# Performance work log

Measured on AMD Instinct MI355X. Metric: run time of the kernel, lower is better.

Reference implementation:

```python
import jax, jax.numpy as jnp
import numpy as np

N = 100000
E = 1600000

def _norms(src, dst):
    ones = jnp.ones(src.shape[0], dtype=jnp.float32)
    out_deg = jax.ops.segment_sum(ones, src, num_segments=N)
    in_deg = jax.ops.segment_sum(ones, dst, num_segments=N)
    # dgl clamps degree to >=1; with self-loops deg>=1 anyway
    out_norm = jax.lax.rsqrt(jnp.clip(out_deg, 1.0))
    in_norm = jax.lax.rsqrt(jnp.clip(in_deg, 1.0))
    return out_norm, in_norm

def _graph_conv(x, W, b, src, dst, out_norm, in_norm):
    h = (x * out_norm[:, None]) @ W          # [N, dout]
    msg = h[src]                              # gather  [E', dout]
    agg = jax.ops.segment_sum(msg, dst, num_segments=N)
    return agg * in_norm[:, None] + b

def setup_inputs() -> dict:
    key = jax.random.key(0)
    ks = jax.random.split(key, 8)
    feat = jax.random.normal(ks[0], (N, 128), dtype=jnp.float32)
    src = jax.random.randint(ks[1], (E,), 0, N, dtype=jnp.int32)
    dst = jax.random.randint(ks[2], (E,), 0, N, dtype=jnp.int32)
    s1 = 1.0 / np.sqrt(128.0)
    W1 = jax.random.uniform(ks[3], (128, 128), jnp.float32, -s1, s1)
    b1 = jnp.zeros((128,), jnp.float32)
    W2 = jax.random.uniform(ks[4], (128, 128), jnp.float32, -s1, s1)
    b2 = jnp.zeros((128,), jnp.float32)
    W3 = jax.random.uniform(ks[5], (128, 64), jnp.float32, -s1, s1)
    b3 = jnp.zeros((64,), jnp.float32)
    return {"feat": feat, "src": src, "dst": dst,
            "W1": W1, "b1": b1, "W2": W2, "b2": b2, "W3": W3, "b3": b3}

def reference(feat, src, dst, W1, b1, W2, b2, W3, b3):
    # dgl.add_self_loop
    loop = jnp.arange(N, dtype=src.dtype)
    s = jnp.concatenate([src, loop])
    d = jnp.concatenate([dst, loop])
    out_norm, in_norm = _norms(s, d)
    # dropout is identity in eval mode (deterministic reference)
    h = jax.nn.relu(_graph_conv(feat, W1, b1, s, d, out_norm, in_norm))
    h = jax.nn.relu(_graph_conv(h, W2, b2, s, d, out_norm, in_norm))
    h = _graph_conv(h, W3, b3, s, d, out_norm, in_norm)
    return h
```

## Files before the change

### kernel.cpp

```cpp
#include <hip/hip_runtime.h>
#include <hip/hip_fp16.h>


#define NFEAT 128
#define BBITS 8
#define BSZ 256
#define EPB 4096

union H8 { float4 f4; __half2 h2[4]; };

using half8v = __attribute__((ext_vector_type(8))) _Float16;
using f32x4  = __attribute__((ext_vector_type(4))) float;

__global__ __launch_bounds__(256) void hist_kernel(const int* __restrict__ src,
                                                   const int* __restrict__ dst,
                                                   int* __restrict__ hist2,
                                                   int NB, int nblk, int nh, int E) {
    __shared__ int hd[512], hs[512];
    const int t = threadIdx.x, b = blockIdx.x;
    for (int u = t; u < 512; u += 256) { hd[u] = 0; hs[u] = 0; }
    __syncthreads();
    const int base4 = b * (EPB / 4);
    #pragma unroll
    for (int j = 0; j < 4; ++j) {
        int i4 = base4 + j * 256 + t;
        int e0 = i4 * 4;
        if (e0 + 3 < E) {
            int4 s = ((const int4*)src)[i4];
            int4 d = ((const int4*)dst)[i4];
            atomicAdd(&hs[s.x >> BBITS], 1); atomicAdd(&hs[s.y >> BBITS], 1);
            atomicAdd(&hs[s.z >> BBITS], 1); atomicAdd(&hs[s.w >> BBITS], 1);
            atomicAdd(&hd[d.x >> BBITS], 1); atomicAdd(&hd[d.y >> BBITS], 1);
            atomicAdd(&hd[d.z >> BBITS], 1); atomicAdd(&hd[d.w >> BBITS], 1);
        } else {
            for (int e = e0; e < E && e < e0 + 4; ++e) {
                atomicAdd(&hs[src[e] >> BBITS], 1);
                atomicAdd(&hd[dst[e] >> BBITS], 1);
            }
        }
    }
    __syncthreads();
    for (int u = t; u < NB; u += 256) {
        hist2[u * nblk + b]      = hd[u];
        hist2[nh + u * nblk + b] = hs[u];
    }
}

__global__ __launch_bounds__(256) void scan1_kernel(int* __restrict__ data,
                                                    int* __restrict__ blk_sum, int n) {
    const int tid = threadIdx.x, lane = tid & 63, wid = tid >> 6;
    const int i2 = blockIdx.x * 256 + tid;
    int a = 0, b = 0;
    if (2 * i2 + 1 < n)      { int2 v = ((const int2*)data)[i2]; a = v.x; b = v.y; }
    else if (2 * i2 < n)     { a = data[2 * i2]; }
    int s = a + b;
    int incl = s;
    #pragma unroll
    for (int off = 1; off < 64; off <<= 1) {
        int t2 = __shfl_up(incl, off, 64);
        if (lane >= off) incl += t2;
    }
    __shared__ int ws[4];
    if (lane == 63) ws[wid] = incl;
    __syncthreads();
    int woff = 0;
    #pragma unroll
    for (int w = 0; w < 3; ++w) if (w < wid) woff += ws[w];
    int pref = woff + incl - s;
    if (2 * i2 < n)     data[2 * i2]     = pref;
    if (2 * i2 + 1 < n) data[2 * i2 + 1] = pref + a;
    if (tid == 0) blk_sum[blockIdx.x] = ws[0] + ws[1] + ws[2] + ws[3];
}

__global__ __launch_bounds__(1024) void scan2_kernel(int* __restrict__ blk, int nb) {
    const int tid = threadIdx.x, lane = tid & 63, wid = tid >> 6;
    int v = (tid < nb) ? blk[tid] : 0;
    int incl = v;
    #pragma unroll
    for (int off = 1; off < 64; off <<= 1) {
        int t = __shfl_up(incl, off, 64);
        if (lane >= off) incl += t;
    }
    __shared__ int ws[16];
    if (lane == 63) ws[wid] = incl;
    __syncthreads();
    int woff = 0;
    #pragma unroll
    for (int w = 0; w < 15; ++w) if (w < wid) woff += ws[w];
    if (tid < nb) blk[tid] = woff + incl - v;
}

__global__ __launch_bounds__(256) void scan3_kernel(int* __restrict__ data,
                                                    const int* __restrict__ blk, int n) {
    const int i2 = blockIdx.x * 256 + threadIdx.x;
    int add = blk[blockIdx.x];
    if (2 * i2 < n)     data[2 * i2]     += add;
    if (2 * i2 + 1 < n) data[2 * i2 + 1] += add;
}

__global__ __launch_bounds__(512) void scatter_kernel(const int* __restrict__ src,
                                                      const int* __restrict__ dst,
                                                      const int* __restrict__ hist2,
                                                      unsigned int* __restrict__ dstP,
                                                      unsigned char* __restrict__ srcB,
                                                      int NB, int nblk, int nh, int E) {
    __shared__ int hd[512], hs[512], startD[512], startS[512], baseD[512], baseS[512];
    __shared__ int ws[8];
    __shared__ unsigned int   payD[EPB];
    __shared__ unsigned short kD[EPB];
    __shared__ unsigned char  sV[EPB];
    __shared__ unsigned short kS[EPB];
    const int t = threadIdx.x, b = blockIdx.x;
    const int lane = t & 63, wid = t >> 6;
    hd[t] = 0; hs[t] = 0;
    for (int u = t; u < NB; u += 512) {
        baseD[u] = hist2[u * nblk + b];
        baseS[u] = hist2[nh + u * nblk + b] - E;
    }
    __syncthreads();

    const int e0 = b * EPB;
    const int nE = min(EPB, E - e0);
    int se[8], de[8], rD[8], rS[8];
    const int be = e0 + t * 8;
    if (be + 7 < E) {
        int4 s0 = ((const int4*)src)[(be >> 2)];
        int4 s1 = ((const int4*)src)[(be >> 2) + 1];
        int4 d0 = ((const int4*)dst)[(be >> 2)];
        int4 d1 = ((const int4*)dst)[(be >> 2) + 1];
        se[0]=s0.x; se[1]=s0.y; se[2]=s0.z; se[3]=s0.w;
        se[4]=s1.x; se[5]=s1.y; se[6]=s1.z; se[7]=s1.w;
        de[0]=d0.x; de[1]=d0.y; de[2]=d0.z; de[3]=d0.w;
        de[4]=d1.x; de[5]=d1.y; de[6]=d1.z; de[7]=d1.w;
    } else {
        #pragma unroll
        for (int j = 0; j < 8; ++j) {
            se[j] = (be + j < E) ? src[be + j] : 0;
            de[j] = (be + j < E) ? dst[be + j] : 0;
        }
    }
    #pragma unroll
    for (int j = 0; j < 8; ++j) {
        if (be + j < E) {
            rD[j] = atomicAdd(&hd[de[j] >> BBITS], 1);
            rS[j] = atomicAdd(&hs[se[j] >> BBITS], 1);
        }
    }
    __syncthreads();
    {
        int v = hd[t], incl = v;
        #pragma unroll
        for (int o = 1; o < 64; o <<= 1) {
            int x = __shfl_up(incl, o, 64);
            if (lane >= o) incl += x;
        }
        if (lane == 63) ws[wid] = incl;
        __syncthreads();
        int woff = 0;
        #pragma unroll
        for (int w = 0; w < 7; ++w) if (w < wid) woff += ws[w];
        startD[t] = woff + incl - v;
    }
    __syncthreads();
    {
        int v = hs[t], incl = v;
        #pragma unroll
        for (int o = 1; o < 64; o <<= 1) {
            int x = __shfl_up(incl, o, 64);
            if (lane >= o) incl += x;
        }
        if (lane == 63) ws[wid] = incl;
        __syncthreads();
        int woff = 0;
        #pragma unroll
        for (int w = 0; w < 7; ++w) if (w < wid) woff += ws[w];
        startS[t] = woff + incl - v;
    }
    __syncthreads();
    #pragma unroll
    for (int j = 0; j < 8; ++j) {
        if (be + j < E) {
            int kd = de[j] >> BBITS;
            int p  = startD[kd] + rD[j];
            payD[p] = ((unsigned int)(de[j] & (BSZ - 1)) << 24) | (unsigned int)se[j];
            kD[p]   = (unsigned short)kd;
            int ks = se[j] >> BBITS;
            int q  = startS[ks] + rS[j];
            sV[q] = (unsigned char)(se[j] & (BSZ - 1));
            kS[q] = (unsigned short)ks;
        }
    }
    __syncthreads();
    for (int p = t; p < nE; p += 512) {
        int k = kD[p];
        dstP[baseD[k] + (p - startD[k])] = payD[p];
        int k2 = kS[p];
        srcB[baseS[k2] + (p - startS[k2])] = sV[p];
    }
}

__global__ __launch_bounds__(256) void bucket_kernel(const unsigned int* __restrict__ dstP,
                                                     const unsigned char* __restrict__ srcB,
                                                     const int* __restrict__ hist2,
                                                     int* __restrict__ row_ptr,
                                                     int* __restrict__ col_idx,
                                                     float* __restrict__ in_norm,
                                                     float* __restrict__ out_norm,
                                                     int N, int NB, int nblk, int nh, int E) {
    __shared__ int cnt[BSZ], scnt[BSZ], start[BSZ], off[BSZ];
    __shared__ int ws[4];
    const int k = blockIdx.x, t = threadIdx.x;
    const int node0 = k << BBITS;
    cnt[t] = 0; scnt[t] = 0; off[t] = 0;
    __syncthreads();
    const int bB = hist2[k * nblk];
    const int bE = (k + 1 < NB) ? hist2[(k + 1) * nblk] : E;
    const int sB = hist2[nh + k * nblk] - E;
    const int sE = ((k + 1 < NB) ? hist2[nh + (k + 1) * nblk] : 2 * E) - E;
    for (int i = bB + t; i < bE; i += 256) atomicAdd(&cnt[dstP[i] >> 24], 1);
    for (int i = sB + t; i < sE; i += 256) atomicAdd(&scnt[srcB[i]], 1);
    __syncthreads();
    const int lane = t & 63, wid = t >> 6;
    int v = cnt[t];
    int incl = v;
    #pragma unroll
    for (int o = 1; o < 64; o <<= 1) {
        int x = __shfl_up(incl, o, 64);
        if (lane >= o) incl += x;
    }
    if (lane == 63) ws[wid] = incl;
    __syncthreads();
    int woff = 0;
    #pragma unroll
    for (int w = 0; w < 3; ++w) if (w < wid) woff += ws[w];
    start[t] = woff + incl - v;
    {
        int node = node0 + t;
        if (node < N) {
            row_ptr[node] = bB + start[t];
            in_norm[node]  = rsqrtf((float)(v + 1));
            out_norm[node] = rsqrtf((float)(scnt[t] + 1));
        }
    }
    if (k == 0 && t == 0) row_ptr[N] = E;
    __syncthreads();
    for (int i = bB + t; i < bE; i += 256) {
        unsigned int pv = dstP[i];
        int local = pv >> 24;
        int r = atomicAdd(&off[local], 1);
        col_idx[bB + start[local] + r] = (int)(pv & 0xFFFFFFu);
    }
}

__global__ void wt_all_kernel(const float* __restrict__ W1, const float* __restrict__ W2,
                              const float* __restrict__ W3, __half* __restrict__ Wt1,
                              __half* __restrict__ Wt2, __half* __restrict__ Wt3) {
    int b = blockIdx.x, k = threadIdx.x;
    if (b < 128)      Wt1[b * 128 + k] = __float2half(W1[k * 128 + b]);
    else if (b < 256) { int n = b - 128; Wt2[n * 128 + k] = __float2half(W2[k * 128 + n]); }
    else              { int n = b - 256; Wt3[n * 128 + k] = __float2half(W3[k * 64 + n]); }
}

template <int BN, typename XT>
__global__ __launch_bounds__(256) void mfma_gemm_kernel(const XT* __restrict__ x,
                                                        const __half* __restrict__ Wt,
                                                        const float* __restrict__ out_norm,
                                                        __half* __restrict__ h, int n_rows) {
    constexpr int BM = 64;
    constexpr int NT = BN / 16;
    __shared__ __half As[BM][136];
    __shared__ __half Bs[BN][136];
    const int tid  = threadIdx.x;
    const int row0 = blockIdx.x * BM;

    {
        int r  = tid >> 2;
        int c0 = (tid & 3) * 32;
        int grow = row0 + r;
        if (grow < n_rows) {
            float norm = out_norm[grow];
            if constexpr (sizeof(XT) == 4) {
                const float* xp = (const float*)x + (size_t)grow * NFEAT + c0;
                #pragma unroll
                for (int j = 0; j < 4; ++j) {
                    float4 p0 = *(const float4*)(xp + j * 8);
                    float4 p1 = *(const float4*)(xp + j * 8 + 4);
                    H8 u;
                    u.h2[0] = __floats2half2_rn(p0.x * norm, p0.y * norm);
                    u.h2[1] = __floats2half2_rn(p0.z * norm, p0.w * norm);
                    u.h2[2] = __floats2half2_rn(p1.x * norm, p1.y * norm);
                    u.h2[3] = __floats2half2_rn(p1.z * norm, p1.w * norm);
                    *(float4*)&As[r][c0 + j * 8] = u.f4;
                }
            } else {
                const __half* xp = (const __half*)x + (size_t)grow * NFEAT + c0;
                #pragma unroll
                for (int j = 0; j < 4; ++j) {
                    H8 u; u.f4 = *(const float4*)(xp + j * 8);
                    #pragma unroll
                    for (int q = 0; q < 4; ++q) {
                        float2 p = __half22float2(u.h2[q]);
                        u.h2[q] = __floats2half2_rn(p.x * norm, p.y * norm);
                    }
                    *(float4*)&As[r][c0 + j * 8] = u.f4;
                }
            }
        } else {
            H8 z; z.f4 = make_float4(0.f, 0.f, 0.f, 0.f);
            #pragma unroll
            for (int j = 0; j < 4; ++j) *(float4*)&As[r][c0 + j * 8] = z.f4;
        }
    }
    {
        constexpr int TPR = 256 / BN;
        constexpr int CH  = 128 / TPR;
        int wr = tid / TPR;
        int wc = (tid % TPR) * CH;
        const __half* wp = Wt + wr * 128 + wc;
        #pragma unroll
        for (int j = 0; j < CH / 8; ++j)
            *(float4*)&Bs[wr][wc + j * 8] = *(const float4*)(wp + j * 8);
    }
    __syncthreads();

    const int lane = tid & 63, wid = tid >> 6;
    const int lr = lane & 15, quad = lane >> 4;
    const int koff = quad * 8;
    f32x4 acc[NT];
    #pragma unroll
    for (int t = 0; t < NT; ++t) acc[t] = (f32x4){0.f, 0.f, 0.f, 0.f};

    #pragma unroll
    for (int ks = 0; ks < 4; ++ks) {
        half8v a = *(const half8v*)&As[wid * 16 + lr][ks * 32 + koff];
        #pragma unroll
        for (int nt = 0; nt < NT; ++nt) {
            half8v b = *(const half8v*)&Bs[nt * 16 + lr][ks * 32 + koff];
            acc[nt] = __builtin_amdgcn_mfma_f32_16x16x32_f16(a, b, acc[nt], 0, 0, 0);
        }
    }

    #pragma unroll
    for (int nt = 0; nt < NT; ++nt) {
        #pragma unroll
        for (int r = 0; r < 4; ++r) {
            int row = row0 + wid * 16 + quad * 4 + r;
            if (row < n_rows)
                h[(size_t)row * BN + nt * 16 + lr] = __float2half(acc[nt][r]);
        }
    }
}

template <int DOUT, bool RELU, typename OutT>
__global__ __launch_bounds__(256) void agg_kernel(const __half* __restrict__ h,
                                                  const int* __restrict__ row_ptr,
                                                  const int* __restrict__ col_idx,
                                                  const float* __restrict__ in_norm,
                                                  const float* __restrict__ bias,
                                                  OutT* __restrict__ out, int n) {
    constexpr int TPN = DOUT / 8;
    constexpr int NPB = 256 / TPN;
    const int tid  = threadIdx.x;
    const int sub  = tid / TPN;
    const int c    = (tid % TPN) * 8;
    const int node = blockIdx.x * NPB + sub;
    if (node >= n) return;

    float acc[8];
    {
        H8 u; u.f4 = *(const float4*)(h + (size_t)node * DOUT + c);
        #pragma unroll
        for (int q = 0; q < 4; ++q) {
            float2 p = __half22float2(u.h2[q]);
            acc[q * 2] = p.x; acc[q * 2 + 1] = p.y;
        }
    }
    int e  = row_ptr[node];
    int e1 = row_ptr[node + 1];
    for (; e + 3 < e1; e += 4) {
        int s0 = col_idx[e], s1 = col_idx[e + 1], s2 = col_idx[e + 2], s3 = col_idx[e + 3];
        H8 u0, u1, u2, u3;
        u0.f4 = *(const float4*)(h + (size_t)s0 * DOUT + c);
        u1.f4 = *(const float4*)(h + (size_t)s1 * DOUT + c);
        u2.f4 = *(const float4*)(h + (size_t)s2 * DOUT + c);
        u3.f4 = *(const float4*)(h + (size_t)s3 * DOUT + c);
        #pragma unroll
        for (int q = 0; q < 4; ++q) {
            float2 p0 = __half22float2(u0.h2[q]);
            float2 p1 = __half22float2(u1.h2[q]);
            float2 p2 = __half22float2(u2.h2[q]);
            float2 p3 = __half22float2(u3.h2[q]);
            acc[q * 2]     += (p0.x + p1.x) + (p2.x + p3.x);
            acc[q * 2 + 1] += (p0.y + p1.y) + (p2.y + p3.y);
        }
    }
    for (; e < e1; ++e) {
        int s0 = col_idx[e];
        H8 u0; u0.f4 = *(const float4*)(h + (size_t)s0 * DOUT + c);
        #pragma unroll
        for (int q = 0; q < 4; ++q) {
            float2 p0 = __half22float2(u0.h2[q]);
            acc[q * 2] += p0.x; acc[q * 2 + 1] += p0.y;
        }
    }
    float inn = in_norm[node];
    float r[8];
    #pragma unroll
    for (int q = 0; q < 8; ++q) {
        r[q] = acc[q] * inn + bias[c + q];
        if (RELU) r[q] = fmaxf(r[q], 0.0f);
    }
    if constexpr (sizeof(OutT) == 2) {
        H8 o;
        #pragma unroll
        for (int q = 0; q < 4; ++q) o.h2[q] = __floats2half2_rn(r[q * 2], r[q * 2 + 1]);
        *(float4*)((__half*)out + (size_t)node * DOUT + c) = o.f4;
    } else {
        float4 o0, o1;
        o0.x=r[0]; o0.y=r[1]; o0.z=r[2]; o0.w=r[3];
        o1.x=r[4]; o1.y=r[5]; o1.z=r[6]; o1.w=r[7];
        *(float4*)((float*)out + (size_t)node * DOUT + c)     = o0;
        *(float4*)((float*)out + (size_t)node * DOUT + c + 4) = o1;
    }
}

extern "C" void kernel_launch(void* const* d_in, const int* in_sizes, int n_in,
                              void* d_out, int out_size, void* d_ws, size_t ws_size,
                              hipStream_t stream) {
    const float* feat = (const float*)d_in[0];
    const int*   src  = (const int*)d_in[1];
    const int*   dst  = (const int*)d_in[2];
    const float* W1   = (const float*)d_in[3];
    const float* b1   = (const float*)d_in[4];
    const float* W2   = (const float*)d_in[5];
    const float* b2   = (const float*)d_in[6];
    const float* W3   = (const float*)d_in[7];
    const float* b3   = (const float*)d_in[8];

    const int N = in_sizes[0] / NFEAT;
    const int E = in_sizes[1];

    const int NB   = (N + BSZ - 1) / BSZ;
    const int nblk = (E + EPB - 1) / EPB;
    const int nh   = NB * nblk;
    const int n2   = 2 * nh;
    const int nsb  = (n2 + 511) / 512;

    char* ws = (char*)d_ws;
    auto alloc = [&](size_t bytes) {
        char* p = ws;
        ws += (bytes + 255) & ~(size_t)255;
        return p;
    };
    float* out_norm = (float*)alloc((size_t)N * 4);
    float* in_norm  = (float*)alloc((size_t)N * 4);
    int*   row_ptr  = (int*)alloc((size_t)(N + 1) * 4);
    int*   hist2    = (int*)alloc((size_t)n2 * 4);
    int*   blk_sum  = (int*)alloc((size_t)1024 * 4);
    __half* Wt1     = (__half*)alloc((size_t)128 * 128 * 2);
    __half* Wt2     = (__half*)alloc((size_t)128 * 128 * 2);
    __half* Wt3     = (__half*)alloc((size_t)64 * 128 * 2);
    int*   col_idx  = (int*)alloc((size_t)E * 4);
    __half* hA      = (__half*)alloc((size_t)N * NFEAT * 2);
    __half* hB      = (__half*)alloc((size_t)N * NFEAT * 2);
    unsigned int*  dstP = (unsigned int*)hA;
    unsigned char* srcB = (unsigned char*)(dstP + E);

    wt_all_kernel<<<320, 128, 0, stream>>>(W1, W2, W3, Wt1, Wt2, Wt3);

    hist_kernel<<<nblk, 256, 0, stream>>>(src, dst, hist2, NB, nblk, nh, E);
    scan1_kernel<<<nsb, 256, 0, stream>>>(hist2, blk_sum, n2);
    scan2_kernel<<<1, 1024, 0, stream>>>(blk_sum, nsb);
    scan3_kernel<<<nsb, 256, 0, stream>>>(hist2, blk_sum, n2);
    scatter_kernel<<<nblk, 512, 0, stream>>>(src, dst, hist2, dstP, srcB, NB, nblk, nh, E);
    bucket_kernel<<<NB, 256, 0, stream>>>(dstP, srcB, hist2, row_ptr, col_idx,
                                          in_norm, out_norm, N, NB, nblk, nh, E);

    const int gb = (N + 63) / 64;
    mfma_gemm_kernel<128, float><<<gb, 256, 0, stream>>>(feat, Wt1, out_norm, hA, N);
    agg_kernel<128, true, __half><<<(N + 15) / 16, 256, 0, stream>>>(hA, row_ptr, col_idx,
                                                                     in_norm, b1, hB, N);
    mfma_gemm_kernel<128, __half><<<gb, 256, 0, stream>>>(hB, Wt2, out_norm, hA, N);
    agg_kernel<128, true, __half><<<(N + 15) / 16, 256, 0, stream>>>(hA, row_ptr, col_idx,
                                                                     in_norm, b2, hB, N);
    mfma_gemm_kernel<64, __half><<<gb, 256, 0, stream>>>(hB, Wt3, out_norm, hA, N);
    agg_kernel<64, false, float><<<(N + 31) / 32, 256, 0, stream>>>(hA, row_ptr, col_idx,
                                                                    in_norm, b3, (float*)d_out, N);
}
```

Baseline: 345.9 us.

## Fuse aggregation of layers 1-2 with the following layer's GEMM

The layer-1 and layer-2 aggregation (gather-sum, norm, bias, ReLU, out_norm scaling) now writes its half-precision result straight into shared memory, and the next layer's MFMA GEMM runs in the same kernel. This removes two launches and the global write and re-read of the intermediate N x 128 activation. In exchange, each fused block handles 64 nodes with 16 threads per node over four serial passes, which may reduce memory-level parallelism for the irregular gathers, and blocks with high-degree nodes can stall the GEMM.

```diff
diff --git a/kernel.cpp b/kernel.cpp
--- a/kernel.cpp
+++ b/kernel.cpp
@@ -261,17 +261,15 @@
     else              { int n = b - 256; Wt3[n * 128 + k] = __float2half(W3[k * 64 + n]); }
 }
 
-template <int BN, typename XT>
-__global__ __launch_bounds__(256) void mfma_gemm_kernel(const XT* __restrict__ x,
+__global__ __launch_bounds__(256) void mfma_gemm_kernel(const float* __restrict__ x,
                                                         const __half* __restrict__ Wt,
                                                         const float* __restrict__ out_norm,
                                                         __half* __restrict__ h, int n_rows) {
-    constexpr int BM = 64;
-    constexpr int NT = BN / 16;
-    __shared__ __half As[BM][136];
+    constexpr int BN = 128, NT = BN / 16;
+    __shared__ __half As[64][136];
     __shared__ __half Bs[BN][136];
     const int tid  = threadIdx.x;
-    const int row0 = blockIdx.x * BM;
+    const int row0 = blockIdx.x * 64;
 
     {
         int r  = tid >> 2;
@@ -279,31 +277,17 @@
         int grow = row0 + r;
         if (grow < n_rows) {
             float norm = out_norm[grow];
-            if constexpr (sizeof(XT) == 4) {
-                const float* xp = (const float*)x + (size_t)grow * NFEAT + c0;
-                #pragma unroll
-                for (int j = 0; j < 4; ++j) {
-                    float4 p0 = *(const float4*)(xp + j * 8);
-                    float4 p1 = *(const float4*)(xp + j * 8 + 4);
-                    H8 u;
-                    u.h2[0] = __floats2half2_rn(p0.x * norm, p0.y * norm);
-                    u.h2[1] = __floats2half2_rn(p0.z * norm, p0.w * norm);
-                    u.h2[2] = __floats2half2_rn(p1.x * norm, p1.y * norm);
-                    u.h2[3] = __floats2half2_rn(p1.z * norm, p1.w * norm);
-                    *(float4*)&As[r][c0 + j * 8] = u.f4;
-                }
-            } else {
-                const __half* xp = (const __half*)x + (size_t)grow * NFEAT + c0;
-                #pragma unroll
-                for (int j = 0; j < 4; ++j) {
-                    H8 u; u.f4 = *(const float4*)(xp + j * 8);
-                    #pragma unroll
-                    for (int q = 0; q < 4; ++q) {
-                        float2 p = __half22float2(u.h2[q]);
-                        u.h2[q] = __floats2half2_rn(p.x * norm, p.y * norm);
-                    }
-                    *(float4*)&As[r][c0 + j * 8] = u.f4;
-                }
+            const float* xp = x + (size_t)grow * NFEAT + c0;
+            #pragma unroll
+            for (int j = 0; j < 4; ++j) {
+                float4 p0 = *(const float4*)(xp + j * 8);
+                float4 p1 = *(const float4*)(xp + j * 8 + 4);
+                H8 u;
+                u.h2[0] = __floats2half2_rn(p0.x * norm, p0.y * norm);
+                u.h2[1] = __floats2half2_rn(p0.z * norm, p0.w * norm);
+                u.h2[2] = __floats2half2_rn(p1.x * norm, p1.y * norm);
+                u.h2[3] = __floats2half2_rn(p1.z * norm, p1.w * norm);
+                *(float4*)&As[r][c0 + j * 8] = u.f4;
             }
         } else {
             H8 z; z.f4 = make_float4(0.f, 0.f, 0.f, 0.f);
@@ -312,6 +296,56 @@
         }
     }
     {
+        int wr = tid / 2;
+        int wc = (tid % 2) * 64;
+        const __half* wp = Wt + wr * 128 + wc;
+        #pragma unroll
+        for (int j = 0; j < 8; ++j)
+            *(float4*)&Bs[wr][wc + j * 8] = *(const float4*)(wp + j * 8);
+    }
+    __syncthreads();
+
+    const int lane = tid & 63, wid = tid >> 6;
+    const int lr = lane & 15, quad = lane >> 4;
+    const int koff = quad * 8;
+    f32x4 acc[NT];
+    #pragma unroll
+    for (int t = 0; t < NT; ++t) acc[t] = (f32x4){0.f, 0.f, 0.f, 0.f};
+
+    #pragma unroll
+    for (int ks = 0; ks < 4; ++ks) {
+        half8v a = *(const half8v*)&As[wid * 16 + lr][ks * 32 + koff];
+        #pragma unroll
+        for (int nt = 0; nt < NT; ++nt) {
+            half8v b = *(const half8v*)&Bs[nt * 16 + lr][ks * 32 + koff];
+            acc[nt] = __builtin_amdgcn_mfma_f32_16x16x32_f16(a, b, acc[nt], 0, 0, 0);
+        }
+    }
+
+    #pragma unroll
+    for (int nt = 0; nt < NT; ++nt) {
+        #pragma unroll
+        for (int r = 0; r < 4; ++r) {
+            int row = row0 + wid * 16 + quad * 4 + r;
+            if (row < n_rows)
+                h[(size_t)row * BN + nt * 16 + lr] = __float2half(acc[nt][r]);
+        }
+    }
+}
+
+template <int BN>
+__global__ __launch_bounds__(256) void fused_agg_gemm_kernel(
+        const __half* __restrict__ hin, const int* __restrict__ row_ptr,
+        const int* __restrict__ col_idx, const float* __restrict__ in_norm,
+        const float* __restrict__ out_norm, const float* __restrict__ bias,
+        const __half* __restrict__ Wt, __half* __restrict__ hout, int n) {
+    constexpr int NT = BN / 16;
+    __shared__ __half As[64][136];
+    __shared__ __half Bs[BN][136];
+    const int tid   = threadIdx.x;
+    const int node0 = blockIdx.x * 64;
+
+    {
         constexpr int TPR = 256 / BN;
         constexpr int CH  = 128 / TPR;
         int wr = tid / TPR;
@@ -321,6 +355,66 @@
         for (int j = 0; j < CH / 8; ++j)
             *(float4*)&Bs[wr][wc + j * 8] = *(const float4*)(wp + j * 8);
     }
+
+    const int sub = tid >> 4;
+    const int c   = (tid & 15) * 8;
+    #pragma unroll
+    for (int p = 0; p < 4; ++p) {
+        const int nl   = p * 16 + sub;
+        const int node = node0 + nl;
+        if (node < n) {
+            float acc[8];
+            {
+                H8 u; u.f4 = *(const float4*)(hin + (size_t)node * 128 + c);
+                #pragma unroll
+                for (int q = 0; q < 4; ++q) {
+                    float2 pp = __half22float2(u.h2[q]);
+                    acc[q * 2] = pp.x; acc[q * 2 + 1] = pp.y;
+                }
+            }
+            int e  = row_ptr[node];
+            int e1 = row_ptr[node + 1];
+            for (; e + 3 < e1; e += 4) {
+                int s0 = col_idx[e], s1 = col_idx[e + 1];
+                int s2 = col_idx[e + 2], s3 = col_idx[e + 3];
+                H8 u0, u1, u2, u3;
+                u0.f4 = *(const float4*)(hin + (size_t)s0 * 128 + c);
+                u1.f4 = *(const float4*)(hin + (size_t)s1 * 128 + c);
+                u2.f4 = *(const float4*)(hin + (size_t)s2 * 128 + c);
+                u3.f4 = *(const float4*)(hin + (size_t)s3 * 128 + c);
+                #pragma unroll
+                for (int q = 0; q < 4; ++q) {
+                    float2 p0 = __half22float2(u0.h2[q]);
+                    float2 p1 = __half22float2(u1.h2[q]);
+                    float2 p2 = __half22float2(u2.h2[q]);
+                    float2 p3 = __half22float2(u3.h2[q]);
+                    acc[q * 2]     += (p0.x + p1.x) + (p2.x + p3.x);
+                    acc[q * 2 + 1] += (p0.y + p1.y) + (p2.y + p3.y);
+                }
+            }
+            for (; e < e1; ++e) {
+                int s0 = col_idx[e];
+                H8 u0; u0.f4 = *(const float4*)(hin + (size_t)s0 * 128 + c);
+                #pragma unroll
+                for (int q = 0; q < 4; ++q) {
+                    float2 p0 = __half22float2(u0.h2[q]);
+                    acc[q * 2] += p0.x; acc[q * 2 + 1] += p0.y;
+                }
+            }
+            float inn = in_norm[node], onorm = out_norm[node];
+            H8 o;
+            #pragma unroll
+            for (int q = 0; q < 4; ++q) {
+                float r0 = fmaxf(acc[q * 2]     * inn + bias[c + q * 2],     0.0f) * onorm;
+                float r1 = fmaxf(acc[q * 2 + 1] * inn + bias[c + q * 2 + 1], 0.0f) * onorm;
+                o.h2[q] = __floats2half2_rn(r0, r1);
+            }
+            *(float4*)&As[nl][c] = o.f4;
+        } else {
+            H8 z; z.f4 = make_float4(0.f, 0.f, 0.f, 0.f);
+            *(float4*)&As[nl][c] = z.f4;
+        }
+    }
     __syncthreads();
 
     const int lane = tid & 63, wid = tid >> 6;
@@ -344,22 +438,20 @@
     for (int nt = 0; nt < NT; ++nt) {
         #pragma unroll
         for (int r = 0; r < 4; ++r) {
-            int row = row0 + wid * 16 + quad * 4 + r;
-            if (row < n_rows)
-                h[(size_t)row * BN + nt * 16 + lr] = __float2half(acc[nt][r]);
-        }
-    }
-}
-
-template <int DOUT, bool RELU, typename OutT>
-__global__ __launch_bounds__(256) void agg_kernel(const __half* __restrict__ h,
-                                                  const int* __restrict__ row_ptr,
-                                                  const int* __restrict__ col_idx,
-                                                  const float* __restrict__ in_norm,
-                                                  const float* __restrict__ bias,
-                                                  OutT* __restrict__ out, int n) {
-    constexpr int TPN = DOUT / 8;
-    constexpr int NPB = 256 / TPN;
+            int row = node0 + wid * 16 + quad * 4 + r;
+            if (row < n)
+                hout[(size_t)row * BN + nt * 16 + lr] = __float2half(acc[nt][r]);
+        }
+    }
+}
+
+__global__ __launch_bounds__(256) void agg64_kernel(const __half* __restrict__ h,
+                                                    const int* __restrict__ row_ptr,
+                                                    const int* __restrict__ col_idx,
+                                                    const float* __restrict__ in_norm,
+                                                    const float* __restrict__ bias,
+                                                    float* __restrict__ out, int n) {
+    constexpr int DOUT = 64, TPN = DOUT / 8, NPB = 256 / TPN;
     const int tid  = threadIdx.x;
     const int sub  = tid / TPN;
     const int c    = (tid % TPN) * 8;
@@ -404,24 +496,13 @@
         }
     }
     float inn = in_norm[node];
-    float r[8];
-    #pragma unroll
-    for (int q = 0; q < 8; ++q) {
-        r[q] = acc[q] * inn + bias[c + q];
-        if (RELU) r[q] = fmaxf(r[q], 0.0f);
-    }
-    if constexpr (sizeof(OutT) == 2) {
-        H8 o;
-        #pragma unroll
-        for (int q = 0; q < 4; ++q) o.h2[q] = __floats2half2_rn(r[q * 2], r[q * 2 + 1]);
-        *(float4*)((__half*)out + (size_t)node * DOUT + c) = o.f4;
-    } else {
-        float4 o0, o1;
-        o0.x=r[0]; o0.y=r[1]; o0.z=r[2]; o0.w=r[3];
-        o1.x=r[4]; o1.y=r[5]; o1.z=r[6]; o1.w=r[7];
-        *(float4*)((float*)out + (size_t)node * DOUT + c)     = o0;
-        *(float4*)((float*)out + (size_t)node * DOUT + c + 4) = o1;
-    }
+    float4 o0, o1;
+    o0.x = acc[0] * inn + bias[c + 0]; o0.y = acc[1] * inn + bias[c + 1];
+    o0.z = acc[2] * inn + bias[c + 2]; o0.w = acc[3] * inn + bias[c + 3];
+    o1.x = acc[4] * inn + bias[c + 4]; o1.y = acc[5] * inn + bias[c + 5];
+    o1.z = acc[6] * inn + bias[c + 6]; o1.w = acc[7] * inn + bias[c + 7];
+    *(float4*)(out + (size_t)node * DOUT + c)     = o0;
+    *(float4*)(out + (size_t)node * DOUT + c + 4) = o1;
 }
 
 extern "C" void kernel_launch(void* const* d_in, const int* in_sizes, int n_in,
@@ -477,13 +558,11 @@
                                           in_norm, out_norm, N, NB, nblk, nh, E);
 
     const int gb = (N + 63) / 64;
-    mfma_gemm_kernel<128, float><<<gb, 256, 0, stream>>>(feat, Wt1, out_norm, hA, N);
-    agg_kernel<128, true, __half><<<(N + 15) / 16, 256, 0, stream>>>(hA, row_ptr, col_idx,
-                                                                     in_norm, b1, hB, N);
-    mfma_gemm_kernel<128, __half><<<gb, 256, 0, stream>>>(hB, Wt2, out_norm, hA, N);
-    agg_kernel<128, true, __half><<<(N + 15) / 16, 256, 0, stream>>>(hA, row_ptr, col_idx,
-                                                                     in_norm, b2, hB, N);
-    mfma_gemm_kernel<64, __half><<<gb, 256, 0, stream>>>(hB, Wt3, out_norm, hA, N);
-    agg_kernel<64, false, float><<<(N + 31) / 32, 256, 0, stream>>>(hA, row_ptr, col_idx,
-                                                                    in_norm, b3, (float*)d_out, N);
-}
+    mfma_gemm_kernel<<<gb, 256, 0, stream>>>(feat, Wt1, out_norm, hA, N);
+    fused_agg_gemm_kernel<128><<<gb, 256, 0, stream>>>(hA, row_ptr, col_idx, in_norm,
+                                                       out_norm, b1, Wt2, hB, N);
+    fused_agg_gemm_kernel<64><<<gb, 256, 0, stream>>>(hB, row_ptr, col_idx, in_norm,
+                                                      out_norm, b2, Wt3, hA, N);
+    agg64_kernel<<<(N + 31) / 32, 256, 0, stream>>>(hA, row_ptr, col_idx, in_norm, b3,
+                                                    (float*)d_out, N);
+}
```

After: 364.8 us. 1.05x slower.
